# Kernel optimization log

Hardware: AMD Instinct MI355X
Metric: run time of the kernel (lower is better)

The kernel has to match this reference:

```python
import jax, jax.numpy as jnp
import numpy as np

N_NODES = 50000
N_EDGES = 800000
IN_DIM = 256
HEADS = 4
HEAD_DIM = 64  # out_dim // heads
NEG_SLOPE = 0.2  # PyG GATConv default


def setup_inputs() -> dict:
    key = jax.random.key(0)
    k1, k2, k3, k4, k5 = jax.random.split(key, 5)
    x = jax.random.normal(k1, (N_NODES, IN_DIM), dtype=jnp.float32)
    edge_index = jax.random.randint(k2, (2, N_EDGES), 0, N_NODES, dtype=jnp.int64)
    # Glorot-ish scaling
    W = jax.random.normal(k3, (IN_DIM, HEADS * HEAD_DIM), dtype=jnp.float32) * (1.0 / np.sqrt(IN_DIM))
    att_src = jax.random.normal(k4, (HEADS, HEAD_DIM), dtype=jnp.float32) * (1.0 / np.sqrt(HEAD_DIM))
    att_dst = jax.random.normal(k5, (HEADS, HEAD_DIM), dtype=jnp.float32) * (1.0 / np.sqrt(HEAD_DIM))
    bias = jnp.zeros((HEADS * HEAD_DIM,), dtype=jnp.float32)
    return {"x": x, "edge_index": edge_index, "W": W, "att_src": att_src,
            "att_dst": att_dst, "bias": bias}


def reference(x, edge_index, W, att_src, att_dst, bias):
    N = x.shape[0]
    # add self-loops (PyG GATConv default)
    loops = jnp.arange(N, dtype=edge_index.dtype)
    src = jnp.concatenate([edge_index[0], loops])
    dst = jnp.concatenate([edge_index[1], loops])

    h = (x @ W).reshape(N, HEADS, HEAD_DIM)          # [N,H,D]
    a_src = jnp.einsum('nhd,hd->nh', h, att_src)     # [N,H]
    a_dst = jnp.einsum('nhd,hd->nh', h, att_dst)     # [N,H]

    e = a_src[src] + a_dst[dst]                      # [E,H]
    e = jax.nn.leaky_relu(e, NEG_SLOPE)

    # segment softmax over edges sharing a destination node
    m = jax.ops.segment_max(e, dst, num_segments=N)  # [N,H]
    e = jnp.exp(e - m[dst])
    denom = jax.ops.segment_sum(e, dst, num_segments=N)  # [N,H]
    alpha = e / denom[dst]                           # [E,H]

    msg = alpha[:, :, None] * h[src]                 # [E,H,D]
    out = jax.ops.segment_sum(msg, dst, num_segments=N)  # [N,H,D]
    return out.reshape(N, HEADS * HEAD_DIM) + bias
```

## Files before the change

kernel.cpp:

```cpp
#include <hip/hip_runtime.h>
#include <hip/hip_bf16.h>

#define N_NODES 50000
#define N_EDGES 800000
#define IN_DIM 256
#define HEADS 4
#define HEAD_DIM 64
#define OUT_DIM 256
#define NEG_SLOPE 0.2f
#define TOTAL_E (N_EDGES + N_NODES)
#define M_PAD 50048
#define SEG_CAP 64

#define GEMM_BLOCKS 782
#define SCAT_BLOCKS 3321
#define MEGA_BLOCKS (GEMM_BLOCKS + SCAT_BLOCKS)

typedef float floatx4 __attribute__((ext_vector_type(4)));
typedef short shortx8 __attribute__((ext_vector_type(8)));

__global__ __launch_bounds__(256) void mega_kernel(const float* __restrict__ x,
                                                   const float* __restrict__ W,
                                                   const float* __restrict__ att_src,
                                                   const float* __restrict__ att_dst,
                                                   const int* __restrict__ e_src,
                                                   const int* __restrict__ e_dst,
                                                   int* __restrict__ cnt,
                                                   int* __restrict__ csr,
                                                   __hip_bfloat16* __restrict__ h2,
                                                   float* __restrict__ asrc,
                                                   float* __restrict__ adst) {
    __shared__ ushort A_lds[64 * 40];
    __shared__ ushort B_lds[256 * 40];

    if (blockIdx.x >= GEMM_BLOCKS) {
        int id = (blockIdx.x - GEMM_BLOCKS) * 256 + threadIdx.x;
        if (id < N_EDGES) {
            int s = e_src[id];
            int dn = e_dst[id];
            int pos = atomicAdd(&cnt[dn], 1);
            if (pos < SEG_CAP) csr[(dn << 6) + pos] = s;
        } else if (id < TOTAL_E) {
            int nn = id - N_EDGES;
            int pos = atomicAdd(&cnt[nn], 1);
            if (pos < SEG_CAP) csr[(nn << 6) + pos] = nn;
        }
        return;
    }

    const int tid = threadIdx.x;
    const int w = tid >> 6;
    const int lane = tid & 63;
    const int quad = lane >> 4;
    const int l16 = lane & 15;
    const int row0 = blockIdx.x * 64;

    floatx4 acc[4][4] = {};

    for (int k0 = 0; k0 < IN_DIM; k0 += 32) {
        {
            int row = tid >> 2, kk = (tid & 3) * 8;
            int gr = row0 + row;
            alignas(16) ushort a8[8];
            if (gr < N_NODES) {
                float4 v0 = *(const float4*)&x[(size_t)gr * IN_DIM + k0 + kk];
                float4 v1 = *(const float4*)&x[(size_t)gr * IN_DIM + k0 + kk + 4];
                float f[8] = {v0.x, v0.y, v0.z, v0.w, v1.x, v1.y, v1.z, v1.w};
#pragma unroll
                for (int j = 0; j < 8; ++j) a8[j] = __bfloat16_as_ushort(__float2bfloat16(f[j]));
            } else {
#pragma unroll
                for (int j = 0; j < 8; ++j) a8[j] = 0;
            }
            *(uint4*)&A_lds[row * 40 + kk] = *(const uint4*)a8;
        }
        {
            int kk = w * 8;
            int kbase = k0 + kk;
#pragma unroll
            for (int c4 = 0; c4 < 4; ++c4) {
                int n = lane + c4 * 64;
                alignas(16) ushort b8[8];
#pragma unroll
                for (int j = 0; j < 8; ++j)
                    b8[j] = __bfloat16_as_ushort(
                        __float2bfloat16(W[(size_t)(kbase + j) * OUT_DIM + n]));
                *(uint4*)&B_lds[n * 40 + kk] = *(const uint4*)b8;
            }
        }
        __syncthreads();
        shortx8 af[4], bf[4];
#pragma unroll
        for (int r = 0; r < 4; ++r)
            af[r] = *(const shortx8*)&A_lds[(r * 16 + l16) * 40 + quad * 8];
#pragma unroll
        for (int c = 0; c < 4; ++c)
            bf[c] = *(const shortx8*)&B_lds[(w * 64 + c * 16 + l16) * 40 + quad * 8];
#pragma unroll
        for (int r = 0; r < 4; ++r)
#pragma unroll
            for (int c = 0; c < 4; ++c)
                acc[r][c] = __builtin_amdgcn_mfma_f32_16x16x32_bf16(af[r], bf[c], acc[r][c], 0, 0, 0);
        __syncthreads();
    }

    float as_c[4], ad_c[4];
#pragma unroll
    for (int c = 0; c < 4; ++c) {
        as_c[c] = att_src[w * 64 + c * 16 + l16];
        ad_c[c] = att_dst[w * 64 + c * 16 + l16];
    }
#pragma unroll
    for (int r = 0; r < 4; ++r) {
        float s[4] = {0.f, 0.f, 0.f, 0.f}, dd[4] = {0.f, 0.f, 0.f, 0.f};
#pragma unroll
        for (int c = 0; c < 4; ++c)
#pragma unroll
            for (int j = 0; j < 4; ++j) {
                s[j] = fmaf(acc[r][c][j], as_c[c], s[j]);
                dd[j] = fmaf(acc[r][c][j], ad_c[c], dd[j]);
            }
#pragma unroll
        for (int m = 1; m <= 8; m <<= 1)
#pragma unroll
            for (int j = 0; j < 4; ++j) {
                s[j] += __shfl_xor(s[j], m);
                dd[j] += __shfl_xor(dd[j], m);
            }
        if (l16 == 0) {
#pragma unroll
            for (int j = 0; j < 4; ++j) {
                int node = row0 + r * 16 + quad * 4 + j;
                if (node < N_NODES) {
                    asrc[node * HEADS + w] = s[j];
                    adst[node * HEADS + w] = dd[j];
                }
            }
        }
#pragma unroll
        for (int c = 0; c < 4; ++c)
#pragma unroll
            for (int j = 0; j < 4; ++j) {
                int node = row0 + r * 16 + quad * 4 + j;
                h2[(size_t)node * OUT_DIM + w * 64 + c * 16 + l16] =
                    __float2bfloat16(acc[r][c][j]);
            }
    }
}

__global__ __launch_bounds__(256) void aggregate_v7(const uint2* __restrict__ h2,
                                                    const float* __restrict__ a_src,
                                                    const float* __restrict__ a_dst,
                                                    const int* __restrict__ cnt,
                                                    const int* __restrict__ csr,
                                                    const float* __restrict__ bias,
                                                    float* __restrict__ out) {
    int n = blockIdx.x * 4 + (threadIdx.x >> 6);
    if (n >= N_NODES) return;
    int lane = threadIdx.x & 63;
    int h = lane >> 4;
    int beg = n << 6;
    int cn = min(cnt[n], SEG_CAP);
    int nfull = cn >> 3, rem = cn & 7;
    float adv = a_dst[n * HEADS + h];

    float den = 0.f;
    float acc0 = 0.f, acc1 = 0.f, acc2 = 0.f, acc3 = 0.f;
    for (int b = 0; b < nfull; ++b) {
        int i = beg + b * 8;
        int4 sa = *(const int4*)&csr[i];
        int4 sb = *(const int4*)&csr[i + 4];
        int ss[8] = {sa.x, sa.y, sa.z, sa.w, sb.x, sb.y, sb.z, sb.w};
        float asv[8];
        uint2 hv[8];
#pragma unroll
        for (int u = 0; u < 8; ++u) {
            asv[u] = a_src[ss[u] * HEADS + h];
            hv[u] = h2[(size_t)ss[u] * 64 + lane];
        }
#pragma unroll
        for (int u = 0; u < 8; ++u) {
            float e = asv[u] + adv;
            e = fmaxf(e, NEG_SLOPE * e);
            float p = __expf(e);
            den += p;
            acc0 = fmaf(p, __uint_as_float(hv[u].x << 16), acc0);
            acc1 = fmaf(p, __uint_as_float(hv[u].x & 0xffff0000u), acc1);
            acc2 = fmaf(p, __uint_as_float(hv[u].y << 16), acc2);
            acc3 = fmaf(p, __uint_as_float(hv[u].y & 0xffff0000u), acc3);
        }
    }
    if (rem) {
        int i = beg + nfull * 8;
        int4 sa = *(const int4*)&csr[i];
        int4 sb = *(const int4*)&csr[i + 4];
        int ss[8] = {sa.x, sa.y, sa.z, sa.w, sb.x, sb.y, sb.z, sb.w};
        float asv[8];
        uint2 hv[8];
#pragma unroll
        for (int u = 0; u < 8; ++u) {
            int s = (u < rem) ? ss[u] : 0;
            asv[u] = a_src[s * HEADS + h];
            hv[u] = h2[(size_t)s * 64 + lane];
        }
#pragma unroll
        for (int u = 0; u < 8; ++u) {
            float e = asv[u] + adv;
            e = fmaxf(e, NEG_SLOPE * e);
            float p = (u < rem) ? __expf(e) : 0.f;
            den += p;
            acc0 = fmaf(p, __uint_as_float(hv[u].x << 16), acc0);
            acc1 = fmaf(p, __uint_as_float(hv[u].x & 0xffff0000u), acc1);
            acc2 = fmaf(p, __uint_as_float(hv[u].y << 16), acc2);
            acc3 = fmaf(p, __uint_as_float(hv[u].y & 0xffff0000u), acc3);
        }
    }
    float idv = 1.0f / den;
    float4 b = *(const float4*)&bias[lane * 4];
    float4 o = make_float4(acc0 * idv + b.x, acc1 * idv + b.y,
                           acc2 * idv + b.z, acc3 * idv + b.w);
    *(float4*)&out[(size_t)n * OUT_DIM + lane * 4] = o;
}

extern "C" void kernel_launch(void* const* d_in, const int* in_sizes, int n_in,
                              void* d_out, int out_size, void* d_ws, size_t ws_size,
                              hipStream_t stream) {
    const float* x = (const float*)d_in[0];
    const int* ei = (const int*)d_in[1];
    const float* W = (const float*)d_in[2];
    const float* att_src = (const float*)d_in[3];
    const float* att_dst = (const float*)d_in[4];
    const float* bias = (const float*)d_in[5];
    float* out = (float*)d_out;

    const int* e_src = ei;
    const int* e_dst = ei + N_EDGES;

    char* p = (char*)d_ws;
    auto alloc = [&](size_t bytes) {
        void* r = (void*)p;
        p += (bytes + 255) & ~(size_t)255;
        return r;
    };
    ushort* h2   = (ushort*)alloc((size_t)M_PAD * OUT_DIM * 2);
    float* asrc  = (float*)alloc((size_t)N_NODES * HEADS * 4);
    float* adst  = (float*)alloc((size_t)N_NODES * HEADS * 4);
    int* cnt     = (int*)alloc((size_t)N_NODES * 4);
    int* csr     = (int*)alloc((size_t)N_NODES * SEG_CAP * 4);

    hipMemsetAsync(cnt, 0, (size_t)N_NODES * 4, stream);
    mega_kernel<<<MEGA_BLOCKS, 256, 0, stream>>>(x, W, att_src, att_dst, e_src, e_dst,
                                                 cnt, csr, (__hip_bfloat16*)h2, asrc, adst);
    aggregate_v7<<<(N_NODES + 3) / 4, 256, 0, stream>>>((const uint2*)h2, asrc, adst,
                                                        cnt, csr, bias, out);
}
```

Measured before the change: 223.9 us.

## Pre-transpose W to bf16 and load GEMM fragments straight from global memory

Adds a small prep kernel that converts W to a transposed bf16 copy, so the GEMM no longer converts W inside every block. The GEMM drops its LDS staging and barriers and loads MFMA fragments directly from global memory, with the MFMA operands swapped so each lane holds contiguous output columns. That lets h2 be written as 16-byte vector stores, and it lets the attention dot products finish with two shuffles instead of four. The aggregate kernel remaps its bias and output columns to match the permuted h2 layout. The cost is an extra launch and uncoalesced-ish direct global fragment loads of x and Wt, which now rely on cache reuse instead of LDS.

```diff
diff --git a/kernel.cpp b/kernel.cpp
--- a/kernel.cpp
+++ b/kernel.cpp
@@ -19,20 +19,30 @@
 typedef float floatx4 __attribute__((ext_vector_type(4)));
 typedef short shortx8 __attribute__((ext_vector_type(8)));
 
+__global__ __launch_bounds__(256) void prep_wt(const float* __restrict__ W,
+                                               ushort* __restrict__ Wt) {
+    int t = blockIdx.x * 256 + threadIdx.x;
+    int n = t >> 6;
+    int k = (t & 63) << 2;
+    ushort4 o;
+    o.x = __bfloat16_as_ushort(__float2bfloat16(W[(size_t)(k + 0) * OUT_DIM + n]));
+    o.y = __bfloat16_as_ushort(__float2bfloat16(W[(size_t)(k + 1) * OUT_DIM + n]));
+    o.z = __bfloat16_as_ushort(__float2bfloat16(W[(size_t)(k + 2) * OUT_DIM + n]));
+    o.w = __bfloat16_as_ushort(__float2bfloat16(W[(size_t)(k + 3) * OUT_DIM + n]));
+    *(ushort4*)&Wt[(size_t)n * IN_DIM + k] = o;
+}
+
 __global__ __launch_bounds__(256) void mega_kernel(const float* __restrict__ x,
-                                                   const float* __restrict__ W,
+                                                   const ushort* __restrict__ Wt,
                                                    const float* __restrict__ att_src,
                                                    const float* __restrict__ att_dst,
                                                    const int* __restrict__ e_src,
                                                    const int* __restrict__ e_dst,
                                                    int* __restrict__ cnt,
                                                    int* __restrict__ csr,
-                                                   __hip_bfloat16* __restrict__ h2,
+                                                   ushort* __restrict__ h2,
                                                    float* __restrict__ asrc,
                                                    float* __restrict__ adst) {
-    __shared__ ushort A_lds[64 * 40];
-    __shared__ ushort B_lds[256 * 40];
-
     if (blockIdx.x >= GEMM_BLOCKS) {
         int id = (blockIdx.x - GEMM_BLOCKS) * 256 + threadIdx.x;
         if (id < N_EDGES) {
@@ -57,98 +67,78 @@
 
     floatx4 acc[4][4] = {};
 
+    const ushort* wtb = Wt + (size_t)(w * 64 + l16) * IN_DIM + quad * 8;
+
+#pragma unroll 2
     for (int k0 = 0; k0 < IN_DIM; k0 += 32) {
-        {
-            int row = tid >> 2, kk = (tid & 3) * 8;
-            int gr = row0 + row;
+        shortx8 bfr[4], af[4];
+#pragma unroll
+        for (int c = 0; c < 4; ++c)
+            bfr[c] = *(const shortx8*)(wtb + (size_t)c * 16 * IN_DIM + k0);
+#pragma unroll
+        for (int r = 0; r < 4; ++r) {
+            int gr = row0 + r * 16 + l16;
             alignas(16) ushort a8[8];
             if (gr < N_NODES) {
-                float4 v0 = *(const float4*)&x[(size_t)gr * IN_DIM + k0 + kk];
-                float4 v1 = *(const float4*)&x[(size_t)gr * IN_DIM + k0 + kk + 4];
+                const float* xp = &x[(size_t)gr * IN_DIM + k0 + quad * 8];
+                float4 v0 = *(const float4*)xp;
+                float4 v1 = *(const float4*)(xp + 4);
                 float f[8] = {v0.x, v0.y, v0.z, v0.w, v1.x, v1.y, v1.z, v1.w};
 #pragma unroll
-                for (int j = 0; j < 8; ++j) a8[j] = __bfloat16_as_ushort(__float2bfloat16(f[j]));
+                for (int u = 0; u < 8; ++u)
+                    a8[u] = __bfloat16_as_ushort(__float2bfloat16(f[u]));
             } else {
 #pragma unroll
-                for (int j = 0; j < 8; ++j) a8[j] = 0;
+                for (int u = 0; u < 8; ++u) a8[u] = 0;
             }
-            *(uint4*)&A_lds[row * 40 + kk] = *(const uint4*)a8;
-        }
-        {
-            int kk = w * 8;
-            int kbase = k0 + kk;
-#pragma unroll
-            for (int c4 = 0; c4 < 4; ++c4) {
-                int n = lane + c4 * 64;
-                alignas(16) ushort b8[8];
-#pragma unroll
-                for (int j = 0; j < 8; ++j)
-                    b8[j] = __bfloat16_as_ushort(
-                        __float2bfloat16(W[(size_t)(kbase + j) * OUT_DIM + n]));
-                *(uint4*)&B_lds[n * 40 + kk] = *(const uint4*)b8;
+            af[r] = *(const shortx8*)a8;
+        }
+#pragma unroll
+        for (int r = 0; r < 4; ++r)
+#pragma unroll
+            for (int c = 0; c < 4; ++c)
+                acc[r][c] = __builtin_amdgcn_mfma_f32_16x16x32_bf16(bfr[c], af[r],
+                                                                    acc[r][c], 0, 0, 0);
+    }
+
+    float as_cj[16], ad_cj[16];
+#pragma unroll
+    for (int c = 0; c < 4; ++c)
+#pragma unroll
+        for (int j = 0; j < 4; ++j) {
+            int col = w * 64 + c * 16 + quad * 4 + j;
+            as_cj[c * 4 + j] = att_src[col];
+            ad_cj[c * 4 + j] = att_dst[col];
+        }
+#pragma unroll
+    for (int r = 0; r < 4; ++r) {
+        float s = 0.f, d = 0.f;
+        alignas(16) ushort o16[16];
+#pragma unroll
+        for (int c = 0; c < 4; ++c)
+#pragma unroll
+            for (int j = 0; j < 4; ++j) {
+                float v = acc[r][c][j];
+                s = fmaf(v, as_cj[c * 4 + j], s);
+                d = fmaf(v, ad_cj[c * 4 + j], d);
+                o16[c * 4 + j] = __bfloat16_as_ushort(__float2bfloat16(v));
             }
-        }
-        __syncthreads();
-        shortx8 af[4], bf[4];
-#pragma unroll
-        for (int r = 0; r < 4; ++r)
-            af[r] = *(const shortx8*)&A_lds[(r * 16 + l16) * 40 + quad * 8];
-#pragma unroll
-        for (int c = 0; c < 4; ++c)
-            bf[c] = *(const shortx8*)&B_lds[(w * 64 + c * 16 + l16) * 40 + quad * 8];
-#pragma unroll
-        for (int r = 0; r < 4; ++r)
-#pragma unroll
-            for (int c = 0; c < 4; ++c)
-                acc[r][c] = __builtin_amdgcn_mfma_f32_16x16x32_bf16(af[r], bf[c], acc[r][c], 0, 0, 0);
-        __syncthreads();
-    }
-
-    float as_c[4], ad_c[4];
-#pragma unroll
-    for (int c = 0; c < 4; ++c) {
-        as_c[c] = att_src[w * 64 + c * 16 + l16];
-        ad_c[c] = att_dst[w * 64 + c * 16 + l16];
-    }
-#pragma unroll
-    for (int r = 0; r < 4; ++r) {
-        float s[4] = {0.f, 0.f, 0.f, 0.f}, dd[4] = {0.f, 0.f, 0.f, 0.f};
-#pragma unroll
-        for (int c = 0; c < 4; ++c)
-#pragma unroll
-            for (int j = 0; j < 4; ++j) {
-                s[j] = fmaf(acc[r][c][j], as_c[c], s[j]);
-                dd[j] = fmaf(acc[r][c][j], ad_c[c], dd[j]);
-            }
-#pragma unroll
-        for (int m = 1; m <= 8; m <<= 1)
-#pragma unroll
-            for (int j = 0; j < 4; ++j) {
-                s[j] += __shfl_xor(s[j], m);
-                dd[j] += __shfl_xor(dd[j], m);
-            }
-        if (l16 == 0) {
-#pragma unroll
-            for (int j = 0; j < 4; ++j) {
-                int node = row0 + r * 16 + quad * 4 + j;
-                if (node < N_NODES) {
-                    asrc[node * HEADS + w] = s[j];
-                    adst[node * HEADS + w] = dd[j];
-                }
-            }
-        }
-#pragma unroll
-        for (int c = 0; c < 4; ++c)
-#pragma unroll
-            for (int j = 0; j < 4; ++j) {
-                int node = row0 + r * 16 + quad * 4 + j;
-                h2[(size_t)node * OUT_DIM + w * 64 + c * 16 + l16] =
-                    __float2bfloat16(acc[r][c][j]);
-            }
-    }
-}
-
-__global__ __launch_bounds__(256) void aggregate_v7(const uint2* __restrict__ h2,
+        s += __shfl_xor(s, 16);
+        s += __shfl_xor(s, 32);
+        d += __shfl_xor(d, 16);
+        d += __shfl_xor(d, 32);
+        int gr = row0 + r * 16 + l16;
+        if (quad == 0 && gr < N_NODES) {
+            asrc[gr * HEADS + w] = s;
+            adst[gr * HEADS + w] = d;
+        }
+        ushort* hp = h2 + (size_t)gr * OUT_DIM + w * 64 + quad * 16;
+        *(uint4*)hp = *(const uint4*)&o16[0];
+        *(uint4*)(hp + 8) = *(const uint4*)&o16[8];
+    }
+}
+
+__global__ __launch_bounds__(256) void aggregate_v8(const uint2* __restrict__ h2,
                                                     const float* __restrict__ a_src,
                                                     const float* __restrict__ a_dst,
                                                     const int* __restrict__ cnt,
@@ -159,6 +149,7 @@
     if (n >= N_NODES) return;
     int lane = threadIdx.x & 63;
     int h = lane >> 4;
+    int col0 = ((lane >> 4) << 6) + ((lane & 3) << 4) + (((lane >> 2) & 3) << 2);
     int beg = n << 6;
     int cn = min(cnt[n], SEG_CAP);
     int nfull = cn >> 3, rem = cn & 7;
@@ -216,10 +207,10 @@
         }
     }
     float idv = 1.0f / den;
-    float4 b = *(const float4*)&bias[lane * 4];
+    float4 b = *(const float4*)&bias[col0];
     float4 o = make_float4(acc0 * idv + b.x, acc1 * idv + b.y,
                            acc2 * idv + b.z, acc3 * idv + b.w);
-    *(float4*)&out[(size_t)n * OUT_DIM + lane * 4] = o;
+    *(float4*)&out[(size_t)n * OUT_DIM + col0] = o;
 }
 
 extern "C" void kernel_launch(void* const* d_in, const int* in_sizes, int n_in,
@@ -247,10 +238,12 @@
     float* adst  = (float*)alloc((size_t)N_NODES * HEADS * 4);
     int* cnt     = (int*)alloc((size_t)N_NODES * 4);
     int* csr     = (int*)alloc((size_t)N_NODES * SEG_CAP * 4);
+    ushort* Wt   = (ushort*)alloc((size_t)IN_DIM * OUT_DIM * 2);
 
     hipMemsetAsync(cnt, 0, (size_t)N_NODES * 4, stream);
-    mega_kernel<<<MEGA_BLOCKS, 256, 0, stream>>>(x, W, att_src, att_dst, e_src, e_dst,
-                                                 cnt, csr, (__hip_bfloat16*)h2, asrc, adst);
-    aggregate_v7<<<(N_NODES + 3) / 4, 256, 0, stream>>>((const uint2*)h2, asrc, adst,
+    prep_wt<<<64, 256, 0, stream>>>(W, Wt);
+    mega_kernel<<<MEGA_BLOCKS, 256, 0, stream>>>(x, Wt, att_src, att_dst, e_src, e_dst,
+                                                 cnt, csr, h2, asrc, adst);
+    aggregate_v8<<<(N_NODES + 3) / 4, 256, 0, stream>>>((const uint2*)h2, asrc, adst,
                                                         cnt, csr, bias, out);
 }
```

Result: slower. 245.9 us (+9.8%).
